# Kernel tuning notes

Hardware: AMD Instinct MI355X
Metric: run time of the kernel (lower is better)

## Reference

```python
import jax, jax.numpy as jnp
import numpy as np

B, S, D = 4096, 200, 64
NUM_USERS = 100000
NUM_ITEMS = 100000


def setup_inputs() -> dict:
    key = jax.random.key(0)
    ks = jax.random.split(key, 16)
    inp = {
        "user_ids": jax.random.randint(ks[0], (B,), 0, NUM_USERS),
        "item_ids": jax.random.randint(ks[1], (B,), 0, NUM_ITEMS),
        "behavior_sequences": jax.random.randint(ks[2], (B, S), 0, NUM_ITEMS),
        # embedding tables
        "user_table": jax.random.normal(ks[3], (NUM_USERS, D), jnp.float32) * 0.02,
        "item_table": jax.random.normal(ks[4], (NUM_ITEMS, D), jnp.float32) * 0.02,
        # attention MLP: Linear(4D, 80) -> ReLU -> Linear(80, 1)
        "att_w1": jax.random.normal(ks[5], (4 * D, 80), jnp.float32) * 0.05,
        "att_b1": jnp.zeros((80,), jnp.float32),
        "att_w2": jax.random.normal(ks[6], (80, 1), jnp.float32) * 0.1,
        "att_b2": jnp.zeros((1,), jnp.float32),
        # predictor MLP: Linear(2D,64)->ReLU->Linear(64,32)->ReLU->Linear(32,1)->Sigmoid
        "pred_w1": jax.random.normal(ks[7], (2 * D, 64), jnp.float32) * 0.08,
        "pred_b1": jnp.zeros((64,), jnp.float32),
        "pred_w2": jax.random.normal(ks[8], (64, 32), jnp.float32) * 0.12,
        "pred_b2": jnp.zeros((32,), jnp.float32),
        "pred_w3": jax.random.normal(ks[9], (32, 1), jnp.float32) * 0.17,
        "pred_b3": jnp.zeros((1,), jnp.float32),
    }
    return inp


def reference(user_ids, item_ids, behavior_sequences,
              user_table, item_table,
              att_w1, att_b1, att_w2, att_b2,
              pred_w1, pred_b1, pred_w2, pred_b2, pred_w3, pred_b3):
    user_emb = user_table[user_ids]                 # (B, D)
    item_emb = item_table[item_ids]                 # (B, D)
    behavior_emb = item_table[behavior_sequences]   # (B, S, D)

    target = item_emb[:, None, :]                   # (B, 1, D) broadcast over S
    product = behavior_emb * target
    subtract = behavior_emb - target
    target_exp = jnp.broadcast_to(target, behavior_emb.shape)
    feats = jnp.concatenate([behavior_emb, target_exp, product, subtract], axis=-1)  # (B, S, 4D)

    h = jax.nn.relu(feats @ att_w1 + att_b1)        # (B, S, 80)
    scores = (h @ att_w2 + att_b2)[..., 0]          # (B, S)
    attn = jax.nn.softmax(scores, axis=1)           # (B, S)

    pooled = jnp.einsum("bsd,bs->bd", behavior_emb, attn)  # (B, D)

    x = jnp.concatenate([user_emb, pooled], axis=-1)        # (B, 2D)
    x = jax.nn.relu(x @ pred_w1 + pred_b1)
    x = jax.nn.relu(x @ pred_w2 + pred_b2)
    out = jax.nn.sigmoid(x @ pred_w3 + pred_b3)             # (B, 1)
    return out
```

## Files before the change

kernel.cpp:

```cpp
#include <hip/hip_runtime.h>
#include <hip/hip_bf16.h>


typedef __attribute__((ext_vector_type(8))) short          bf16x8;
typedef __attribute__((ext_vector_type(8))) unsigned short u16x8;
typedef __attribute__((ext_vector_type(4))) float          f32x4;

__device__ __forceinline__ int swz_gran(int row, int g) {
    return row * 64 + ((g ^ (row & 7)) << 3);
}
__device__ __forceinline__ int swz_elem(int row, int col) {
    return row * 64 + (((col >> 3) ^ (row & 7)) << 3) + (col & 7);
}
__device__ __forceinline__ float bits2f(unsigned int u) {
    union { unsigned int u; float f; } v; v.u = u; return v.f;
}
__device__ __forceinline__ float bfelem(bf16x8 v, int e) {
    return bits2f(((unsigned int)(unsigned short)v[e]) << 16);
}

extern "C" __global__ __launch_bounds__(256)
void din_prep(const int* __restrict__ item_ids,
              const float* __restrict__ item_table,
              const float* __restrict__ att_w1,
              const float* __restrict__ att_b1,
              __hip_bfloat16* __restrict__ gcb,
              float* __restrict__ bias_out)
{
    const int t = threadIdx.x;
    if (blockIdx.x == 64) {
        for (int i = t; i < 64 * 80; i += 256) {
            const int d = i / 80;
            const int j = i - d * 80;
            const float g = att_w1[d * 80 + j] + att_w1[(192 + d) * 80 + j];
            const float c = att_w1[(128 + d) * 80 + j];
            gcb[swz_elem(j, d)]        = __float2bfloat16(g);
            gcb[5120 + swz_elem(j, d)] = __float2bfloat16(c);
        }
        return;
    }
    __shared__ float wdiff[64 * 80];
    __shared__ float tgts[64 * 64];
    const int b0 = blockIdx.x * 64;
    for (int i = t; i < 64 * 80; i += 256) {
        const int d = i / 80;
        const int j = i - d * 80;
        wdiff[i] = att_w1[(64 + d) * 80 + j] - att_w1[(192 + d) * 80 + j];
    }
    for (int i = t; i < 64 * 64; i += 256) {
        const int bl = i >> 6, d = i & 63;
        tgts[i] = item_table[(size_t)item_ids[b0 + bl] * 64 + d];
    }
    __syncthreads();
    for (int i = t; i < 64 * 80; i += 256) {
        const int bl = i / 80;
        const int j  = i - bl * 80;
        float acc = att_b1[j];
        #pragma unroll 8
        for (int d = 0; d < 64; ++d)
            acc = fmaf(tgts[bl * 64 + d], wdiff[d * 80 + j], acc);
        bias_out[(size_t)(b0 + bl) * 80 + j] = acc;
    }
}

struct __align__(16) LdsW {
    unsigned short gcb[10240];
    float w2[80];
    float biasw[4][80];
    float wsc[4][208];
    float aux[4][128];
    float h1s[4][64];
};

extern "C" __global__ __launch_bounds__(256, 4)
void din_main(const int* __restrict__ user_ids,
              const int* __restrict__ item_ids,
              const int* __restrict__ seq,
              const float* __restrict__ user_table,
              const float* __restrict__ item_table,
              const float* __restrict__ att_w2,
              const float* __restrict__ pred_w1,
              const float* __restrict__ pred_b1,
              const float* __restrict__ pred_w2,
              const float* __restrict__ pred_b2,
              const float* __restrict__ pred_w3,
              const float* __restrict__ pred_b3,
              const unsigned short* __restrict__ gcb_g,
              const float* __restrict__ bias_g,
              float* __restrict__ out)
{
    __shared__ LdsW L;
    const int t  = threadIdx.x;
    const int wv = t >> 6;
    const int l  = t & 63;
    const int lr = l & 15;
    const int ks = l >> 4;
    const int b  = blockIdx.x * 4 + wv;

    {
        const u16x8* src = reinterpret_cast<const u16x8*>(gcb_g);
        u16x8* dst = reinterpret_cast<u16x8*>(L.gcb);
        #pragma unroll
        for (int i = 0; i < 5; ++i) dst[t + i * 256] = src[t + i * 256];
    }
    if (t < 80) L.w2[t] = att_w2[t];
    L.biasw[wv][l] = bias_g[(size_t)b * 80 + l];
    if (l < 16) L.biasw[wv][64 + l] = bias_g[(size_t)b * 80 + 64 + l];

    const int iid = item_ids[b];
    const float4* tp = reinterpret_cast<const float4*>(
        item_table + (size_t)iid * 64);
    const float4 tg0 = tp[2 * ks], tg1 = tp[2 * ks + 1];
    const float4 tg2 = tp[8 + 2 * ks], tg3 = tp[8 + 2 * ks + 1];
    const int uid = user_ids[b];
    const float uem = user_table[(size_t)uid * 64 + l];
    const int* seqb = seq + b * 200;

    __syncthreads();

    float bias_r[5], w2_r[5];
    #pragma unroll
    for (int nt = 0; nt < 5; ++nt) {
        bias_r[nt] = L.biasw[wv][nt * 16 + lr];
        w2_r[nt]   = L.w2[nt * 16 + lr];
    }

    float pl[8], ph[8];
    #pragma unroll
    for (int e = 0; e < 8; ++e) { pl[e] = 0.f; ph[e] = 0.f; }
    float mrun = -1e30f, ssum = 0.f;

    for (int mt = 0; mt < 13; ++mt) {
        const int srow = mt * 16 + lr;
        const bool val = srow < 200;
        const int row = val ? seqb[srow] : 0;
        const float4* rp = reinterpret_cast<const float4*>(
            item_table + (size_t)row * 64);
        float4 q0 = rp[2 * ks], q1 = rp[2 * ks + 1];
        float4 q2 = rp[8 + 2 * ks], q3 = rp[8 + 2 * ks + 1];
        if (!val) {
            q0 = make_float4(0.f, 0.f, 0.f, 0.f);
            q1 = make_float4(0.f, 0.f, 0.f, 0.f);
            q2 = make_float4(0.f, 0.f, 0.f, 0.f);
            q3 = make_float4(0.f, 0.f, 0.f, 0.f);
        }
        union { u16x8 u; bf16x8 bf; __hip_bfloat162 h2[4]; } A0, A1, A2, A3;
        A0.h2[0] = __float22bfloat162_rn(float2{q0.x, q0.y});
        A0.h2[1] = __float22bfloat162_rn(float2{q0.z, q0.w});
        A0.h2[2] = __float22bfloat162_rn(float2{q1.x, q1.y});
        A0.h2[3] = __float22bfloat162_rn(float2{q1.z, q1.w});
        A1.h2[0] = __float22bfloat162_rn(float2{q2.x, q2.y});
        A1.h2[1] = __float22bfloat162_rn(float2{q2.z, q2.w});
        A1.h2[2] = __float22bfloat162_rn(float2{q3.x, q3.y});
        A1.h2[3] = __float22bfloat162_rn(float2{q3.z, q3.w});
        A2.h2[0] = __float22bfloat162_rn(float2{q0.x * tg0.x, q0.y * tg0.y});
        A2.h2[1] = __float22bfloat162_rn(float2{q0.z * tg0.z, q0.w * tg0.w});
        A2.h2[2] = __float22bfloat162_rn(float2{q1.x * tg1.x, q1.y * tg1.y});
        A2.h2[3] = __float22bfloat162_rn(float2{q1.z * tg1.z, q1.w * tg1.w});
        A3.h2[0] = __float22bfloat162_rn(float2{q2.x * tg2.x, q2.y * tg2.y});
        A3.h2[1] = __float22bfloat162_rn(float2{q2.z * tg2.z, q2.w * tg2.w});
        A3.h2[2] = __float22bfloat162_rn(float2{q3.x * tg3.x, q3.y * tg3.y});
        A3.h2[3] = __float22bfloat162_rn(float2{q3.z * tg3.z, q3.w * tg3.w});

        f32x4 acc[5];
        #pragma unroll
        for (int nt = 0; nt < 5; ++nt)
            acc[nt] = (f32x4){0.f, 0.f, 0.f, 0.f};
        #pragma unroll
        for (int nt = 0; nt < 5; ++nt) {
            const int j = nt * 16 + lr;
            const bf16x8 g0 = *reinterpret_cast<const bf16x8*>(
                &L.gcb[swz_gran(j, ks)]);
            const bf16x8 g1 = *reinterpret_cast<const bf16x8*>(
                &L.gcb[swz_gran(j, 4 + ks)]);
            const bf16x8 c0 = *reinterpret_cast<const bf16x8*>(
                &L.gcb[5120 + swz_gran(j, ks)]);
            const bf16x8 c1 = *reinterpret_cast<const bf16x8*>(
                &L.gcb[5120 + swz_gran(j, 4 + ks)]);
            acc[nt] = __builtin_amdgcn_mfma_f32_16x16x32_bf16(A0.bf, g0, acc[nt], 0, 0, 0);
            acc[nt] = __builtin_amdgcn_mfma_f32_16x16x32_bf16(A1.bf, g1, acc[nt], 0, 0, 0);
            acc[nt] = __builtin_amdgcn_mfma_f32_16x16x32_bf16(A2.bf, c0, acc[nt], 0, 0, 0);
            acc[nt] = __builtin_amdgcn_mfma_f32_16x16x32_bf16(A3.bf, c1, acc[nt], 0, 0, 0);
        }

        float pv[4];
        #pragma unroll
        for (int r = 0; r < 4; ++r) {
            const int s = mt * 16 + ks * 4 + r;
            float p = 0.f;
            #pragma unroll
            for (int nt = 0; nt < 5; ++nt)
                p += fmaxf(acc[nt][r] + bias_r[nt], 0.f) * w2_r[nt];
            p += __shfl_xor(p, 1);
            p += __shfl_xor(p, 2);
            p += __shfl_xor(p, 4);
            p += __shfl_xor(p, 8);
            if (s >= 200) p = -1e30f;
            pv[r] = p;
            if (lr == 0 && s < 200) L.wsc[wv][s] = p;
        }
        float tmax = fmaxf(fmaxf(pv[0], pv[1]), fmaxf(pv[2], pv[3]));
        tmax = fmaxf(tmax, __shfl_xor(tmax, 16));
        tmax = fmaxf(tmax, __shfl_xor(tmax, 32));
        if (tmax > mrun) {
            const float sc = __expf(mrun - tmax);
            #pragma unroll
            for (int e = 0; e < 8; ++e) { pl[e] *= sc; ph[e] *= sc; }
            ssum *= sc;
            mrun = tmax;
        }
        float w = 0.f;
        if (val) w = __expf(L.wsc[wv][srow] - mrun);
        ssum += w;
        #pragma unroll
        for (int e = 0; e < 8; ++e) {
            pl[e] = fmaf(w, bfelem(A0.bf, e), pl[e]);
            ph[e] = fmaf(w, bfelem(A1.bf, e), ph[e]);
        }
    }

    #pragma unroll
    for (int msk = 1; msk < 16; msk <<= 1) {
        #pragma unroll
        for (int e = 0; e < 8; ++e) {
            pl[e] += __shfl_xor(pl[e], msk);
            ph[e] += __shfl_xor(ph[e], msk);
        }
        ssum += __shfl_xor(ssum, msk);
    }
    const float inv = 1.f / ssum;
    if (lr == 0) {
        #pragma unroll
        for (int e = 0; e < 8; ++e) {
            L.aux[wv][64 + 8 * ks + e]      = pl[e] * inv;
            L.aux[wv][64 + 32 + 8 * ks + e] = ph[e] * inv;
        }
    }
    L.aux[wv][l] = uem;

    float a0 = pred_b1[l], a1 = 0.f, a2 = 0.f, a3 = 0.f;
    #pragma unroll 4
    for (int k = 0; k < 128; k += 4) {
        a0 = fmaf(L.aux[wv][k],     pred_w1[k * 64 + l],       a0);
        a1 = fmaf(L.aux[wv][k + 1], pred_w1[(k + 1) * 64 + l], a1);
        a2 = fmaf(L.aux[wv][k + 2], pred_w1[(k + 2) * 64 + l], a2);
        a3 = fmaf(L.aux[wv][k + 3], pred_w1[(k + 3) * 64 + l], a3);
    }
    L.h1s[wv][l] = fmaxf((a0 + a1) + (a2 + a3), 0.f);
    const int j2 = l & 31;
    float c0 = pred_b2[j2], c1 = 0.f;
    #pragma unroll 4
    for (int k = 0; k < 64; k += 2) {
        c0 = fmaf(L.h1s[wv][k],     pred_w2[k * 32 + j2],       c0);
        c1 = fmaf(L.h1s[wv][k + 1], pred_w2[(k + 1) * 32 + j2], c1);
    }
    float p = fmaxf(c0 + c1, 0.f) * pred_w3[j2];
    p += __shfl_xor(p, 1);
    p += __shfl_xor(p, 2);
    p += __shfl_xor(p, 4);
    p += __shfl_xor(p, 8);
    p += __shfl_xor(p, 16);
    if (l == 0) {
        const float z = p + pred_b3[0];
        out[b] = 1.f / (1.f + __expf(-z));
    }
}

extern "C" void kernel_launch(void* const* d_in, const int* in_sizes, int n_in,
                              void* d_out, int out_size, void* d_ws, size_t ws_size,
                              hipStream_t stream)
{
    const int*   user_ids   = (const int*)  d_in[0];
    const int*   item_ids   = (const int*)  d_in[1];
    const int*   seq        = (const int*)  d_in[2];
    const float* user_table = (const float*)d_in[3];
    const float* item_table = (const float*)d_in[4];
    const float* att_w1     = (const float*)d_in[5];
    const float* att_b1     = (const float*)d_in[6];
    const float* att_w2     = (const float*)d_in[7];
    const float* pred_w1    = (const float*)d_in[9];
    const float* pred_b1    = (const float*)d_in[10];
    const float* pred_w2    = (const float*)d_in[11];
    const float* pred_b2    = (const float*)d_in[12];
    const float* pred_w3    = (const float*)d_in[13];
    const float* pred_b3    = (const float*)d_in[14];
    float* out = (float*)d_out;

    __hip_bfloat16* gcb = (__hip_bfloat16*)d_ws;
    float* bias_ws = (float*)((char*)d_ws + 20480);

    din_prep<<<65, 256, 0, stream>>>(item_ids, item_table, att_w1, att_b1,
                                     gcb, bias_ws);
    din_main<<<1024, 256, 0, stream>>>(user_ids, item_ids, seq,
                                       user_table, item_table, att_w2,
                                       pred_w1, pred_b1, pred_w2, pred_b2,
                                       pred_w3, pred_b3,
                                       (const unsigned short*)gcb, bias_ws,
                                       out);
}
```

Before: 75.08 us.

## Prefetch next behavior-row gather and spread prep kernel over more blocks

The main kernel now loads all 13 sequence indices up front. Each loop iteration issues the item_table gather for the next tile while the current tile is being processed, so the random-access global load latency can overlap with MFMA and softmax work. Attention pooling now accumulates the original fp32 values instead of re-expanding the bf16-converted copies. The prep kernel handles 16 batch rows per block with 257 blocks instead of 64 rows with 65 blocks, which adds parallelism there. The cost is more live registers from the index array and the second set of float4 buffers, which may lower occupancy.

```diff
diff --git a/kernel.cpp b/kernel.cpp
--- a/kernel.cpp
+++ b/kernel.cpp
@@ -11,12 +11,6 @@
 }
 __device__ __forceinline__ int swz_elem(int row, int col) {
     return row * 64 + (((col >> 3) ^ (row & 7)) << 3) + (col & 7);
-}
-__device__ __forceinline__ float bits2f(unsigned int u) {
-    union { unsigned int u; float f; } v; v.u = u; return v.f;
-}
-__device__ __forceinline__ float bfelem(bf16x8 v, int e) {
-    return bits2f(((unsigned int)(unsigned short)v[e]) << 16);
 }
 
 extern "C" __global__ __launch_bounds__(256)
@@ -28,7 +22,7 @@
               float* __restrict__ bias_out)
 {
     const int t = threadIdx.x;
-    if (blockIdx.x == 64) {
+    if (blockIdx.x == 256) {
         for (int i = t; i < 64 * 80; i += 256) {
             const int d = i / 80;
             const int j = i - d * 80;
@@ -40,19 +34,19 @@
         return;
     }
     __shared__ float wdiff[64 * 80];
-    __shared__ float tgts[64 * 64];
-    const int b0 = blockIdx.x * 64;
+    __shared__ float tgts[16 * 64];
+    const int b0 = blockIdx.x * 16;
     for (int i = t; i < 64 * 80; i += 256) {
         const int d = i / 80;
         const int j = i - d * 80;
         wdiff[i] = att_w1[(64 + d) * 80 + j] - att_w1[(192 + d) * 80 + j];
     }
-    for (int i = t; i < 64 * 64; i += 256) {
+    for (int i = t; i < 16 * 64; i += 256) {
         const int bl = i >> 6, d = i & 63;
         tgts[i] = item_table[(size_t)item_ids[b0 + bl] * 64 + d];
     }
     __syncthreads();
-    for (int i = t; i < 64 * 80; i += 256) {
+    for (int i = t; i < 16 * 80; i += 256) {
         const int bl = i / 80;
         const int j  = i - bl * 80;
         float acc = att_b1[j];
@@ -116,6 +110,21 @@
     const float uem = user_table[(size_t)uid * 64 + l];
     const int* seqb = seq + b * 200;
 
+    int rows[13];
+    #pragma unroll
+    for (int mt = 0; mt < 13; ++mt) {
+        const int srow = mt * 16 + lr;
+        rows[mt] = (srow < 200) ? seqb[srow] : -1;
+    }
+    float4 q0, q1, q2, q3;
+    {
+        const int r0 = rows[0] < 0 ? 0 : rows[0];
+        const float4* rp = reinterpret_cast<const float4*>(
+            item_table + (size_t)r0 * 64);
+        q0 = rp[2 * ks]; q1 = rp[2 * ks + 1];
+        q2 = rp[8 + 2 * ks]; q3 = rp[8 + 2 * ks + 1];
+    }
+
     __syncthreads();
 
     float bias_r[5], w2_r[5];
@@ -130,20 +139,17 @@
     for (int e = 0; e < 8; ++e) { pl[e] = 0.f; ph[e] = 0.f; }
     float mrun = -1e30f, ssum = 0.f;
 
+    #pragma unroll
     for (int mt = 0; mt < 13; ++mt) {
-        const int srow = mt * 16 + lr;
-        const bool val = srow < 200;
-        const int row = val ? seqb[srow] : 0;
-        const float4* rp = reinterpret_cast<const float4*>(
-            item_table + (size_t)row * 64);
-        float4 q0 = rp[2 * ks], q1 = rp[2 * ks + 1];
-        float4 q2 = rp[8 + 2 * ks], q3 = rp[8 + 2 * ks + 1];
-        if (!val) {
-            q0 = make_float4(0.f, 0.f, 0.f, 0.f);
-            q1 = make_float4(0.f, 0.f, 0.f, 0.f);
-            q2 = make_float4(0.f, 0.f, 0.f, 0.f);
-            q3 = make_float4(0.f, 0.f, 0.f, 0.f);
-        }
+        float4 n0, n1, n2, n3;
+        if (mt < 12) {
+            const int rn = rows[mt + 1] < 0 ? 0 : rows[mt + 1];
+            const float4* rp = reinterpret_cast<const float4*>(
+                item_table + (size_t)rn * 64);
+            n0 = rp[2 * ks]; n1 = rp[2 * ks + 1];
+            n2 = rp[8 + 2 * ks]; n3 = rp[8 + 2 * ks + 1];
+        }
+
         union { u16x8 u; bf16x8 bf; __hip_bfloat162 h2[4]; } A0, A1, A2, A3;
         A0.h2[0] = __float22bfloat162_rn(float2{q0.x, q0.y});
         A0.h2[1] = __float22bfloat162_rn(float2{q0.z, q0.w});
@@ -210,13 +216,18 @@
             mrun = tmax;
         }
         float w = 0.f;
-        if (val) w = __expf(L.wsc[wv][srow] - mrun);
+        if (rows[mt] >= 0) w = __expf(L.wsc[wv][mt * 16 + lr] - mrun);
         ssum += w;
-        #pragma unroll
-        for (int e = 0; e < 8; ++e) {
-            pl[e] = fmaf(w, bfelem(A0.bf, e), pl[e]);
-            ph[e] = fmaf(w, bfelem(A1.bf, e), ph[e]);
-        }
+        pl[0] = fmaf(w, q0.x, pl[0]); pl[1] = fmaf(w, q0.y, pl[1]);
+        pl[2] = fmaf(w, q0.z, pl[2]); pl[3] = fmaf(w, q0.w, pl[3]);
+        pl[4] = fmaf(w, q1.x, pl[4]); pl[5] = fmaf(w, q1.y, pl[5]);
+        pl[6] = fmaf(w, q1.z, pl[6]); pl[7] = fmaf(w, q1.w, pl[7]);
+        ph[0] = fmaf(w, q2.x, ph[0]); ph[1] = fmaf(w, q2.y, ph[1]);
+        ph[2] = fmaf(w, q2.z, ph[2]); ph[3] = fmaf(w, q2.w, ph[3]);
+        ph[4] = fmaf(w, q3.x, ph[4]); ph[5] = fmaf(w, q3.y, ph[5]);
+        ph[6] = fmaf(w, q3.z, ph[6]); ph[7] = fmaf(w, q3.w, ph[7]);
+
+        q0 = n0; q1 = n1; q2 = n2; q3 = n3;
     }
 
     #pragma unroll
@@ -289,8 +300,8 @@
     __hip_bfloat16* gcb = (__hip_bfloat16*)d_ws;
     float* bias_ws = (float*)((char*)d_ws + 20480);
 
-    din_prep<<<65, 256, 0, stream>>>(item_ids, item_table, att_w1, att_b1,
-                                     gcb, bias_ws);
+    din_prep<<<257, 256, 0, stream>>>(item_ids, item_table, att_w1, att_b1,
+                                      gcb, bias_ws);
     din_main<<<1024, 256, 0, stream>>>(user_ids, item_ids, seq,
                                        user_table, item_table, att_w2,
                                        pred_w1, pred_b1, pred_w2, pred_b2,
```

After: 146.7 us. +95.4%, slower.

## Fold per-batch attention bias into main kernel via MFMA, drop bias workspace

Applied to the files above, without the earlier changes.

Moves the per-sample bias computation (target embedding times the W_b-W_d weight difference plus b1) out of the prep kernel and into the main kernel. There it is computed with two bf16 MFMAs per output tile, using a third weight block now staged in LDS. This turns the prep kernel into a trivial weight-conversion pass and removes the bias workspace round-trip. The pooling accumulation now uses the fp32 behavior rows instead of the bf16-converted ones. In exchange, LDS use grows, the bias is now computed with bf16 precision, and each block does extra MFMA work.

```diff
diff --git a/kernel.cpp b/kernel.cpp
--- a/kernel.cpp
+++ b/kernel.cpp
@@ -12,61 +12,29 @@
 __device__ __forceinline__ int swz_elem(int row, int col) {
     return row * 64 + (((col >> 3) ^ (row & 7)) << 3) + (col & 7);
 }
-__device__ __forceinline__ float bits2f(unsigned int u) {
-    union { unsigned int u; float f; } v; v.u = u; return v.f;
-}
-__device__ __forceinline__ float bfelem(bf16x8 v, int e) {
-    return bits2f(((unsigned int)(unsigned short)v[e]) << 16);
-}
 
 extern "C" __global__ __launch_bounds__(256)
-void din_prep(const int* __restrict__ item_ids,
-              const float* __restrict__ item_table,
-              const float* __restrict__ att_w1,
-              const float* __restrict__ att_b1,
-              __hip_bfloat16* __restrict__ gcb,
-              float* __restrict__ bias_out)
+void din_prep(const float* __restrict__ att_w1,
+              __hip_bfloat16* __restrict__ gcb)
 {
-    const int t = threadIdx.x;
-    if (blockIdx.x == 64) {
-        for (int i = t; i < 64 * 80; i += 256) {
-            const int d = i / 80;
-            const int j = i - d * 80;
-            const float g = att_w1[d * 80 + j] + att_w1[(192 + d) * 80 + j];
-            const float c = att_w1[(128 + d) * 80 + j];
-            gcb[swz_elem(j, d)]        = __float2bfloat16(g);
-            gcb[5120 + swz_elem(j, d)] = __float2bfloat16(c);
-        }
-        return;
-    }
-    __shared__ float wdiff[64 * 80];
-    __shared__ float tgts[64 * 64];
-    const int b0 = blockIdx.x * 64;
-    for (int i = t; i < 64 * 80; i += 256) {
+    const int i = blockIdx.x * 256 + threadIdx.x;
+    if (i < 64 * 80) {
         const int d = i / 80;
         const int j = i - d * 80;
-        wdiff[i] = att_w1[(64 + d) * 80 + j] - att_w1[(192 + d) * 80 + j];
-    }
-    for (int i = t; i < 64 * 64; i += 256) {
-        const int bl = i >> 6, d = i & 63;
-        tgts[i] = item_table[(size_t)item_ids[b0 + bl] * 64 + d];
-    }
-    __syncthreads();
-    for (int i = t; i < 64 * 80; i += 256) {
-        const int bl = i / 80;
-        const int j  = i - bl * 80;
-        float acc = att_b1[j];
-        #pragma unroll 8
-        for (int d = 0; d < 64; ++d)
-            acc = fmaf(tgts[bl * 64 + d], wdiff[d * 80 + j], acc);
-        bias_out[(size_t)(b0 + bl) * 80 + j] = acc;
+        const float wa = att_w1[d * 80 + j];
+        const float wb = att_w1[(64 + d) * 80 + j];
+        const float wc = att_w1[(128 + d) * 80 + j];
+        const float wd = att_w1[(192 + d) * 80 + j];
+        const int sw = swz_elem(j, d);
+        gcb[sw]         = __float2bfloat16(wa + wd);
+        gcb[5120 + sw]  = __float2bfloat16(wc);
+        gcb[10240 + sw] = __float2bfloat16(wb - wd);
     }
 }
 
 struct __align__(16) LdsW {
-    unsigned short gcb[10240];
+    unsigned short gcb[15360];
     float w2[80];
-    float biasw[4][80];
     float wsc[4][208];
     float aux[4][128];
     float h1s[4][64];
@@ -78,6 +46,7 @@
               const int* __restrict__ seq,
               const float* __restrict__ user_table,
               const float* __restrict__ item_table,
+              const float* __restrict__ att_b1,
               const float* __restrict__ att_w2,
               const float* __restrict__ pred_w1,
               const float* __restrict__ pred_b1,
@@ -86,7 +55,6 @@
               const float* __restrict__ pred_w3,
               const float* __restrict__ pred_b3,
               const unsigned short* __restrict__ gcb_g,
-              const float* __restrict__ bias_g,
               float* __restrict__ out)
 {
     __shared__ LdsW L;
@@ -100,12 +68,9 @@
     {
         const u16x8* src = reinterpret_cast<const u16x8*>(gcb_g);
         u16x8* dst = reinterpret_cast<u16x8*>(L.gcb);
-        #pragma unroll
-        for (int i = 0; i < 5; ++i) dst[t + i * 256] = src[t + i * 256];
+        for (int i = t; i < 1920; i += 256) dst[i] = src[i];
     }
     if (t < 80) L.w2[t] = att_w2[t];
-    L.biasw[wv][l] = bias_g[(size_t)b * 80 + l];
-    if (l < 16) L.biasw[wv][64 + l] = bias_g[(size_t)b * 80 + 64 + l];
 
     const int iid = item_ids[b];
     const float4* tp = reinterpret_cast<const float4*>(
@@ -119,10 +84,29 @@
     __syncthreads();
 
     float bias_r[5], w2_r[5];
-    #pragma unroll
-    for (int nt = 0; nt < 5; ++nt) {
-        bias_r[nt] = L.biasw[wv][nt * 16 + lr];
-        w2_r[nt]   = L.w2[nt * 16 + lr];
+    {
+        union { u16x8 u; bf16x8 bf; __hip_bfloat162 h2[4]; } T0, T1;
+        T0.h2[0] = __float22bfloat162_rn(float2{tg0.x, tg0.y});
+        T0.h2[1] = __float22bfloat162_rn(float2{tg0.z, tg0.w});
+        T0.h2[2] = __float22bfloat162_rn(float2{tg1.x, tg1.y});
+        T0.h2[3] = __float22bfloat162_rn(float2{tg1.z, tg1.w});
+        T1.h2[0] = __float22bfloat162_rn(float2{tg2.x, tg2.y});
+        T1.h2[1] = __float22bfloat162_rn(float2{tg2.z, tg2.w});
+        T1.h2[2] = __float22bfloat162_rn(float2{tg3.x, tg3.y});
+        T1.h2[3] = __float22bfloat162_rn(float2{tg3.z, tg3.w});
+        #pragma unroll
+        for (int nt = 0; nt < 5; ++nt) {
+            const int j = nt * 16 + lr;
+            const bf16x8 wd0 = *reinterpret_cast<const bf16x8*>(
+                &L.gcb[10240 + swz_gran(j, ks)]);
+            const bf16x8 wd1 = *reinterpret_cast<const bf16x8*>(
+                &L.gcb[10240 + swz_gran(j, 4 + ks)]);
+            f32x4 bacc = (f32x4){0.f, 0.f, 0.f, 0.f};
+            bacc = __builtin_amdgcn_mfma_f32_16x16x32_bf16(T0.bf, wd0, bacc, 0, 0, 0);
+            bacc = __builtin_amdgcn_mfma_f32_16x16x32_bf16(T1.bf, wd1, bacc, 0, 0, 0);
+            bias_r[nt] = bacc[0] + att_b1[j];
+            w2_r[nt]   = L.w2[j];
+        }
     }
 
     float pl[8], ph[8];
@@ -212,11 +196,14 @@
         float w = 0.f;
         if (val) w = __expf(L.wsc[wv][srow] - mrun);
         ssum += w;
-        #pragma unroll
-        for (int e = 0; e < 8; ++e) {
-            pl[e] = fmaf(w, bfelem(A0.bf, e), pl[e]);
-            ph[e] = fmaf(w, bfelem(A1.bf, e), ph[e]);
-        }
+        pl[0] = fmaf(w, q0.x, pl[0]); pl[1] = fmaf(w, q0.y, pl[1]);
+        pl[2] = fmaf(w, q0.z, pl[2]); pl[3] = fmaf(w, q0.w, pl[3]);
+        pl[4] = fmaf(w, q1.x, pl[4]); pl[5] = fmaf(w, q1.y, pl[5]);
+        pl[6] = fmaf(w, q1.z, pl[6]); pl[7] = fmaf(w, q1.w, pl[7]);
+        ph[0] = fmaf(w, q2.x, ph[0]); ph[1] = fmaf(w, q2.y, ph[1]);
+        ph[2] = fmaf(w, q2.z, ph[2]); ph[3] = fmaf(w, q2.w, ph[3]);
+        ph[4] = fmaf(w, q3.x, ph[4]); ph[5] = fmaf(w, q3.y, ph[5]);
+        ph[6] = fmaf(w, q3.z, ph[6]); ph[7] = fmaf(w, q3.w, ph[7]);
     }
 
     #pragma unroll
@@ -287,14 +274,13 @@
     float* out = (float*)d_out;
 
     __hip_bfloat16* gcb = (__hip_bfloat16*)d_ws;
-    float* bias_ws = (float*)((char*)d_ws + 20480);
-
-    din_prep<<<65, 256, 0, stream>>>(item_ids, item_table, att_w1, att_b1,
-                                     gcb, bias_ws);
+
+    din_prep<<<40, 256, 0, stream>>>(att_w1, gcb);
     din_main<<<1024, 256, 0, stream>>>(user_ids, item_ids, seq,
-                                       user_table, item_table, att_w2,
+                                       user_table, item_table,
+                                       att_b1, att_w2,
                                        pred_w1, pred_b1, pred_w2, pred_b2,
                                        pred_w3, pred_b3,
-                                       (const unsigned short*)gcb, bias_ws,
+                                       (const unsigned short*)gcb,
                                        out);
 }
```

After: 63.22 us. 15.8% less time.
